# Optimization experiments

Measured on AMD Instinct MI355X. Metric: run time of the kernel, lower is better.

## Reference

```python
import jax, jax.numpy as jnp
import numpy as np

# Model dims
B, S, H, NH = 2, 2048, 1024, 8
HD = H // NH            # head_dim = 128
T = S * NH              # MoE input tokens per batch = 16384
E, K, F = 8, 2, 512     # experts, top_k, expert FFN dim (4*head_dim)


def setup_inputs() -> dict:
    key = jax.random.key(0)
    ks = jax.random.split(key, 9)
    s = 0.02  # init scale
    return {
        "x": jax.random.normal(ks[0], (B, S, H), jnp.float32),
        "W_mh": jax.random.normal(ks[1], (H, H), jnp.float32) * s,
        "b_mh": jnp.zeros((H,), jnp.float32),
        "W_merge": jax.random.normal(ks[2], (H, H), jnp.float32) * s,
        "b_merge": jnp.zeros((H,), jnp.float32),
        "W_router": jax.random.normal(ks[3], (HD, E), jnp.float32) * s,
        "W1": jax.random.normal(ks[4], (E, HD, F), jnp.float32) * s,
        "b1": jnp.zeros((E, F), jnp.float32),
        "W2": jax.random.normal(ks[5], (E, F, HD), jnp.float32) * s,
        "b2": jnp.zeros((E, HD), jnp.float32),
    }


def reference(x, W_mh, b_mh, W_merge, b_merge, W_router, W1, b1, W2, b2):
    # multi-head projection then split heads into the token axis
    h = x @ W_mh + b_mh                       # [B, S, H]
    h = h.reshape(B, T, HD)                   # [B, T, HD]

    # nested VectorizedMoE: top-k token-choice routing over head_dim tokens
    logits = h @ W_router                     # [B, T, E]
    probs = jax.nn.softmax(logits, axis=-1)
    topv, topi = jax.lax.top_k(probs, K)      # [B, T, K]
    topv = topv / jnp.sum(topv, axis=-1, keepdims=True)  # renormalize top-k gates
    # scatter top-k gates into dense [B, T, E] combine weights
    gates = jnp.sum(jax.nn.one_hot(topi, E, dtype=h.dtype) * topv[..., None], axis=-2)

    # vectorized expert FFNs (all experts, combined with sparse gates)
    a = jax.nn.gelu(jnp.einsum('btd,edf->btef', h, W1) + b1)   # [B, T, E, F]
    y = jnp.einsum('btef,efd->bted', a, W2) + b2               # [B, T, E, HD]
    moe_out = jnp.einsum('bte,bted->btd', gates, y)            # [B, T, HD]

    # merge heads back and final projection
    out = moe_out.reshape(B, S, H) @ W_merge + b_merge         # [B, S, H]
    return out
```

## Files before the change

kernel.cpp:

```cpp
#include <hip/hip_runtime.h>


typedef __attribute__((ext_vector_type(8))) short bf16x8;
typedef __attribute__((ext_vector_type(4))) float f32x4;
typedef __attribute__((ext_vector_type(16))) float f32x16;
typedef __attribute__((ext_vector_type(4))) unsigned short u16x4;

constexpr int NSLOT = 66560;
constexpr int NTILE_MAX = 520;
#define CTRL_CNT 0
#define CTRL_CUR 8

__device__ __forceinline__ unsigned short f2bf(float x) {
  unsigned int u = __float_as_uint(x);
  return (unsigned short)((u + 0x7FFFu + ((u >> 16) & 1u)) >> 16);
}
__device__ __forceinline__ float bf2f(unsigned short u) {
  return __uint_as_float(((unsigned int)u) << 16);
}
__device__ __forceinline__ void gload_lds16(const void* g, void* l) {
  __builtin_amdgcn_global_load_lds(
      (const __attribute__((address_space(1))) unsigned int*)g,
      (__attribute__((address_space(3))) unsigned int*)l, 16, 0, 0);
}

__global__ __launch_bounds__(256) void prep_all(
    const float* __restrict__ x, unsigned short* __restrict__ x_bf,
    const float* __restrict__ Wmh, unsigned short* __restrict__ Wmh_t,
    const float* __restrict__ Wmg, unsigned short* __restrict__ Wmg_t,
    const float* __restrict__ W1, const float* __restrict__ W2,
    unsigned short* __restrict__ W1F, unsigned short* __restrict__ W2F,
    const float* __restrict__ bmh, const float* __restrict__ Wr,
    float* __restrict__ Wc, int* __restrict__ ctrl) {
  __shared__ float smem[2048];
  const int bid = blockIdx.x, tid = threadIdx.x;
  if (bid < 1024) {
    if (bid == 0 && tid < 16) ctrl[tid] = 0;
    int i = bid * 256 + tid;
    const int n4 = 4096 * 1024 / 4, stride = 1024 * 256;
    for (; i < n4; i += stride) {
      float4 v = ((const float4*)x)[i];
      u16x4 o;
      o.x = f2bf(v.x); o.y = f2bf(v.y); o.z = f2bf(v.z); o.w = f2bf(v.w);
      ((u16x4*)x_bf)[i] = o;
    }
  } else if (bid < 3072) {
    const int b = bid - 1024;
    const float* src = (b < 1024) ? Wmh : Wmg;
    unsigned short* dst = (b < 1024) ? Wmh_t : Wmg_t;
    const int bb = b & 1023;
    const int c0 = (bb & 31) * 32, r0 = (bb >> 5) * 32;
    const int tx = tid & 31, ty = tid >> 5;
    float (*tile)[33] = (float(*)[33])smem;
    for (int i = ty; i < 32; i += 8)
      tile[i][tx] = src[(size_t)(r0 + i) * 1024 + c0 + tx];
    __syncthreads();
    for (int i = ty; i < 32; i += 8)
      dst[(size_t)(c0 + i) * 1024 + r0 + tx] = f2bf(tile[tx][i]);
  } else if (bid < 3584) {
    const int jid = (bid - 3072) * 4 + (tid >> 6);
    const int l = tid & 63;
    const int is2 = jid >= 1024;
    const int bj = is2 ? jid - 1024 : jid;
    const float* src;
    int C;
    if (!is2) {
      int kk = bj & 7, ft = (bj >> 3) & 15, e = bj >> 7;
      src = W1 + (size_t)e * 65536 + (size_t)(kk * 16) * 512 + ft * 32;
      C = 512;
    } else {
      int sht = bj & 7, ft = (bj >> 3) & 15, e = bj >> 7;
      src = W2 + (size_t)e * 65536 + (size_t)(ft * 32 + (sht >> 2) * 16) * 128 + (sht & 3) * 32;
      C = 128;
    }
    float* tile = smem + (tid >> 6) * 512;
#pragma unroll
    for (int r = 0; r < 8; ++r) {
      int i = l + 64 * r;
      tile[(i >> 5) * 32 + (i & 31)] = src[(size_t)(i >> 5) * C + (i & 31)];
    }
    __syncthreads();
    int l31 = l & 31, lh = l >> 5;
    bf16x8 v;
#pragma unroll
    for (int j = 0; j < 8; ++j) v[j] = (short)f2bf(tile[(lh * 8 + j) * 32 + l31]);
    unsigned short* dst = is2 ? W2F : W1F;
    *(bf16x8*)(dst + ((size_t)bj * 64 + l) * 8) = v;
  } else {
    const int r = (bid - 3584) * 4 + (tid >> 6);
    if (r > 1024) return;
    const int l = tid & 63;
    const float* src = (r < 1024) ? (Wmh + (size_t)r * 1024) : bmh;
    int nh = l >> 3, e = l & 7;
    float acc = 0.f;
    for (int d = 0; d < 128; ++d) acc = fmaf(src[nh * 128 + d], Wr[d * 8 + e], acc);
    Wc[(size_t)r * 64 + l] = acc;
  }
}

__global__ __launch_bounds__(256) void router_kernel(
    const float* __restrict__ x, const float* __restrict__ Wc,
    int* __restrict__ tok_e, float* __restrict__ tok_g,
    int* __restrict__ ctrl, int* __restrict__ perm, float* __restrict__ gateb) {
  int gi = blockIdx.x * 256 + threadIdx.x;
  if (gi < NSLOT) { perm[gi] = 0; gateb[gi] = 0.f; }

  __shared__ float xs[8 * 1024];
  __shared__ float lg[8][64];
  __shared__ int lcnt[8];
  if (threadIdx.x < 8) lcnt[threadIdx.x] = 0;
  int r0 = blockIdx.x * 8;
  const float4* xg = (const float4*)(x + (size_t)r0 * 1024);
  float4* xs4 = (float4*)xs;
  for (int i = threadIdx.x; i < 2048; i += 256) xs4[i] = xg[i];
  __syncthreads();
  int g = threadIdx.x >> 6, lane = threadIdx.x & 63;
  float a0 = Wc[1024 * 64 + lane], a1 = a0;
  const float* x0 = xs + g * 1024;
  const float* x1 = xs + (g + 4) * 1024;
  for (int k = 0; k < 1024; ++k) {
    float w = Wc[(size_t)k * 64 + lane];
    a0 = fmaf(x0[k], w, a0);
    a1 = fmaf(x1[k], w, a1);
  }
  lg[g][lane] = a0; lg[g + 4][lane] = a1;
  __syncthreads();
  if (threadIdx.x < 64) {
    int row = threadIdx.x >> 3, nh = threadIdx.x & 7;
    float l[8];
#pragma unroll
    for (int e = 0; e < 8; ++e) l[e] = lg[row][nh * 8 + e];
    int i1 = 0; float v1 = l[0];
#pragma unroll
    for (int e = 1; e < 8; ++e) if (l[e] > v1) { v1 = l[e]; i1 = e; }
    int i2 = -1; float v2 = -1e30f;
#pragma unroll
    for (int e = 0; e < 8; ++e) if (e != i1 && l[e] > v2) { v2 = l[e]; i2 = e; }
    float g1 = 1.f / (1.f + __expf(v2 - v1));
    float g2 = 1.f - g1;
    size_t t = (size_t)(r0 + row) * 8 + nh;
    tok_e[t * 2] = i1; tok_e[t * 2 + 1] = i2;
    tok_g[t * 2] = g1; tok_g[t * 2 + 1] = g2;
    atomicAdd(&lcnt[i1], 1);
    atomicAdd(&lcnt[i2], 1);
  }
  __syncthreads();
  if (threadIdx.x < 8 && lcnt[threadIdx.x])
    atomicAdd(&ctrl[CTRL_CNT + threadIdx.x], lcnt[threadIdx.x]);
}

__global__ __launch_bounds__(256) void assign_kernel(
    const int* __restrict__ tok_e, const float* __restrict__ tok_g,
    int* __restrict__ ctrl, int* __restrict__ perm,
    float* __restrict__ gateb, int* __restrict__ tok_slot) {
  __shared__ int lcnt[8], lbase[8];
  if (threadIdx.x < 8) lcnt[threadIdx.x] = 0;
  __syncthreads();
  int t = blockIdx.x * 256 + threadIdx.x;
  int e0 = tok_e[t * 2], e1 = tok_e[t * 2 + 1];
  int p0 = atomicAdd(&lcnt[e0], 1);
  int p1 = atomicAdd(&lcnt[e1], 1);
  __syncthreads();
  if (threadIdx.x < 8)
    lbase[threadIdx.x] = atomicAdd(&ctrl[CTRL_CUR + threadIdx.x], lcnt[threadIdx.x]);
  __syncthreads();
  int off0 = 0, off1 = 0, acc = 0;
#pragma unroll
  for (int i = 0; i < 8; ++i) {
    int cnt = ctrl[CTRL_CNT + i];
    if (i == e0) off0 = acc;
    if (i == e1) off1 = acc;
    acc += (cnt + 127) & ~127;
  }
  int s0 = off0 + lbase[e0] + p0;
  int s1 = off1 + lbase[e1] + p1;
  perm[s0] = t; perm[s1] = t;
  gateb[s0] = tok_g[t * 2]; gateb[s1] = tok_g[t * 2 + 1];
  tok_slot[t * 2] = s0; tok_slot[t * 2 + 1] = s1;
}

template <int OUT_BF16>
__global__ __launch_bounds__(256) void gemm_bt(
    const unsigned short* __restrict__ A, const unsigned short* __restrict__ Bt,
    const float* __restrict__ bias, void* __restrict__ Cout,
    int M, int N, int K) {
  __shared__ unsigned short As[2][64 * 64];
  __shared__ unsigned short Bs[2][128 * 64];
  const int tid = threadIdx.x, lane = tid & 63, wid = tid >> 6;
  const int wr = wid & 1, wc = wid >> 1;
  const int m0 = blockIdx.x * 64, n0 = blockIdx.y * 128;
  const int l15 = lane & 15, lhi = lane >> 4;

  f32x4 acc[2][4];
#pragma unroll
  for (int n = 0; n < 4; ++n) {
    float bv = bias[n0 + wc * 64 + n * 16 + l15];
#pragma unroll
    for (int m = 0; m < 2; ++m) acc[m][n] = (f32x4){bv, bv, bv, bv};
  }

  const int rowi = tid >> 3;
  const int segi = (tid & 7) * 8;
  const int NT = K >> 6;

  auto stage = [&](int buf, int kt) {
    const int k0 = kt * 64;
#pragma unroll
    for (int r = 0; r < 2; ++r)
      gload_lds16(A + (size_t)(m0 + r * 32 + rowi) * K + k0 + segi,
                  &As[buf][r * 2048 + wid * 512]);
#pragma unroll
    for (int r = 0; r < 4; ++r)
      gload_lds16(Bt + (size_t)(n0 + r * 32 + rowi) * K + k0 + segi,
                  &Bs[buf][r * 2048 + wid * 512]);
  };

  stage(0, 0);
  asm volatile("s_waitcnt vmcnt(0)" ::: "memory");
  __syncthreads();
  int cur = 0;
  for (int t = 0; t < NT; ++t) {
    if (t + 1 < NT) stage(cur ^ 1, t + 1);
#pragma unroll
    for (int ks = 0; ks < 64; ks += 32) {
      bf16x8 af[2], bb[4];
#pragma unroll
      for (int m = 0; m < 2; ++m)
        af[m] = *(const bf16x8*)&As[cur][(wr * 32 + m * 16 + l15) * 64 + ks + lhi * 8];
#pragma unroll
      for (int n = 0; n < 4; ++n)
        bb[n] = *(const bf16x8*)&Bs[cur][(wc * 64 + n * 16 + l15) * 64 + ks + lhi * 8];
#pragma unroll
      for (int m = 0; m < 2; ++m)
#pragma unroll
        for (int n = 0; n < 4; ++n)
          acc[m][n] = __builtin_amdgcn_mfma_f32_16x16x32_bf16(af[m], bb[n], acc[m][n], 0, 0, 0);
    }
    asm volatile("s_waitcnt vmcnt(0)" ::: "memory");
    __syncthreads();
    cur ^= 1;
  }
#pragma unroll
  for (int m = 0; m < 2; ++m) {
#pragma unroll
    for (int n = 0; n < 4; ++n) {
      int col = n0 + wc * 64 + n * 16 + l15;
#pragma unroll
      for (int j = 0; j < 4; ++j) {
        int row = m0 + wr * 32 + m * 16 + lhi * 4 + j;
        if (OUT_BF16)
          ((unsigned short*)Cout)[(size_t)row * N + col] = f2bf(acc[m][n][j]);
        else
          ((float*)Cout)[(size_t)row * N + col] = acc[m][n][j];
      }
    }
  }
}

__global__ __launch_bounds__(256, 2) void ffn_sparse_v5(
    const unsigned short* __restrict__ hbf,
    const int* __restrict__ ctrl,
    const int* __restrict__ perm,
    const float* __restrict__ gateb,
    const unsigned short* __restrict__ W1F,
    const float* __restrict__ b1,
    const unsigned short* __restrict__ W2F,
    const float* __restrict__ b2,
    unsigned short* __restrict__ ybuf) {
  int e = -1, slotbase = 0;
  {
    int accT = 0, accS = 0;
#pragma unroll
    for (int i = 0; i < 8; ++i) {
      int cnt = ctrl[CTRL_CNT + i];
      int tiles = (cnt + 127) >> 7;
      if (e < 0 && (int)blockIdx.x < accT + tiles) {
        e = i;
        slotbase = accS + ((int)blockIdx.x - accT) * 128;
      }
      accT += tiles;
      accS += tiles * 128;
    }
  }
  if (e < 0) return;

  const int tid = threadIdx.x, l = tid & 63, w = tid >> 6;
  const int l31 = l & 31, lh = l >> 5;
  const int slot = slotbase + w * 32 + l31;
  const int prow = perm[slot];
  const float gate = gateb[slot];

  bf16x8 hreg[8];
  const unsigned short* hsrc = hbf + (size_t)prow * 128 + lh * 8;
#pragma unroll
  for (int kk = 0; kk < 8; ++kk)
    hreg[kk] = *(const bf16x8*)(hsrc + kk * 16);

  const unsigned short* W1e = W1F + (size_t)e * 65536 + l * 8;
  const unsigned short* W2e = W2F + (size_t)e * 65536 + l * 8;
  const float4* b14 = (const float4*)(b1 + (size_t)e * 512);

  f32x16 yacc[4] = {};
  for (int it = 0; it < 8; ++it) {
    bf16x8 w1c[16], w2a[8], w2b[8];
#pragma unroll
    for (int i = 0; i < 16; ++i)
      w1c[i] = *(const bf16x8*)(W1e + (size_t)it * 8192 + i * 512);
#pragma unroll
    for (int i = 0; i < 8; ++i)
      w2a[i] = *(const bf16x8*)(W2e + (size_t)it * 8192 + i * 512);
    float4 p0 = b14[it * 16 + lh],     p1 = b14[it * 16 + lh + 2];
    float4 p2 = b14[it * 16 + lh + 4], p3 = b14[it * 16 + lh + 6];
    float4 q0 = b14[it * 16 + 8 + lh],     q1 = b14[it * 16 + 8 + lh + 2];
    float4 q2 = b14[it * 16 + 8 + lh + 4], q3 = b14[it * 16 + 8 + lh + 6];
    f32x16 a0 = {p0.x, p0.y, p0.z, p0.w, p1.x, p1.y, p1.z, p1.w,
                 p2.x, p2.y, p2.z, p2.w, p3.x, p3.y, p3.z, p3.w};
    f32x16 a1 = {q0.x, q0.y, q0.z, q0.w, q1.x, q1.y, q1.z, q1.w,
                 q2.x, q2.y, q2.z, q2.w, q3.x, q3.y, q3.z, q3.w};
#pragma unroll
    for (int kk = 0; kk < 8; ++kk) {
      a0 = __builtin_amdgcn_mfma_f32_32x32x16_bf16(w1c[kk], hreg[kk], a0, 0, 0, 0);
      a1 = __builtin_amdgcn_mfma_f32_32x32x16_bf16(w1c[8 + kk], hreg[kk], a1, 0, 0, 0);
    }
#pragma unroll
    for (int i = 0; i < 8; ++i)
      w2b[i] = *(const bf16x8*)(W2e + (size_t)it * 8192 + 4096 + i * 512);
    float ge0[16], ge1[16];
#pragma unroll
    for (int r = 0; r < 16; ++r) {
      float v = a0[r];
      float s2 = v * v;
      float q = fmaf(0.1029432f, s2, 2.3022078f);
      float E = exp2f(v * q);
      float rc = __builtin_amdgcn_rcpf(E + 1.f);
      ge0[r] = fmaf(-v, rc, v) * gate;
      float v1 = a1[r];
      float s21 = v1 * v1;
      float q1v = fmaf(0.1029432f, s21, 2.3022078f);
      float E1 = exp2f(v1 * q1v);
      float rc1 = __builtin_amdgcn_rcpf(E1 + 1.f);
      ge1[r] = fmaf(-v1, rc1, v1) * gate;
    }
    unsigned pk0[8], pk1[8];
#pragma unroll
    for (int p = 0; p < 8; ++p) {
      unsigned r0v, r1v;
      asm("v_cvt_pk_bf16_f32 %0, %1, %2" : "=v"(r0v) : "v"(ge0[2 * p]), "v"(ge0[2 * p + 1]));
      asm("v_cvt_pk_bf16_f32 %0, %1, %2" : "=v"(r1v) : "v"(ge1[2 * p]), "v"(ge1[2 * p + 1]));
      pk0[p] = r0v; pk1[p] = r1v;
    }
    asm volatile("v_permlane32_swap_b32 %0, %1" : "+v"(pk0[0]), "+v"(pk0[2]));
    asm volatile("v_permlane32_swap_b32 %0, %1" : "+v"(pk0[1]), "+v"(pk0[3]));
    asm volatile("v_permlane32_swap_b32 %0, %1" : "+v"(pk0[4]), "+v"(pk0[6]));
    asm volatile("v_permlane32_swap_b32 %0, %1" : "+v"(pk0[5]), "+v"(pk0[7]));
    asm volatile("v_permlane32_swap_b32 %0, %1" : "+v"(pk1[0]), "+v"(pk1[2]));
    asm volatile("v_permlane32_swap_b32 %0, %1" : "+v"(pk1[1]), "+v"(pk1[3]));
    asm volatile("v_permlane32_swap_b32 %0, %1" : "+v"(pk1[4]), "+v"(pk1[6]));
    asm volatile("v_permlane32_swap_b32 %0, %1" : "+v"(pk1[5]), "+v"(pk1[7]));
    typedef __attribute__((ext_vector_type(4))) unsigned u32x4;
    u32x4 f00 = {pk0[0], pk0[1], pk0[2], pk0[3]};
    u32x4 f01 = {pk0[4], pk0[5], pk0[6], pk0[7]};
    u32x4 f10 = {pk1[0], pk1[1], pk1[2], pk1[3]};
    u32x4 f11 = {pk1[4], pk1[5], pk1[6], pk1[7]};
    bf16x8 act00 = __builtin_bit_cast(bf16x8, f00);
    bf16x8 act01 = __builtin_bit_cast(bf16x8, f01);
    bf16x8 act10 = __builtin_bit_cast(bf16x8, f10);
    bf16x8 act11 = __builtin_bit_cast(bf16x8, f11);
#pragma unroll
    for (int ht = 0; ht < 4; ++ht) {
      yacc[ht] = __builtin_amdgcn_mfma_f32_32x32x16_bf16(w2a[ht], act00, yacc[ht], 0, 0, 0);
      yacc[ht] = __builtin_amdgcn_mfma_f32_32x32x16_bf16(w2a[4 + ht], act01, yacc[ht], 0, 0, 0);
      yacc[ht] = __builtin_amdgcn_mfma_f32_32x32x16_bf16(w2b[ht], act10, yacc[ht], 0, 0, 0);
      yacc[ht] = __builtin_amdgcn_mfma_f32_32x32x16_bf16(w2b[4 + ht], act11, yacc[ht], 0, 0, 0);
    }
  }
  const float* b2e = b2 + (size_t)e * 128;
#pragma unroll
  for (int ht = 0; ht < 4; ++ht) {
#pragma unroll
    for (int rp = 0; rp < 8; ++rp) {
      int fr = ((2 * rp) & 3) + 8 * (rp >> 1) + 4 * lh;
      int hd = ht * 32 + fr;
      float2 bb2 = *(const float2*)&b2e[hd];
      float v0 = fmaf(gate, bb2.x, yacc[ht][2 * rp]);
      float v1 = fmaf(gate, bb2.y, yacc[ht][2 * rp + 1]);
      unsigned pw;
      asm("v_cvt_pk_bf16_f32 %0, %1, %2" : "=v"(pw) : "v"(v0), "v"(v1));
      *(unsigned*)(ybuf + (size_t)slot * 128 + hd) = pw;
    }
  }
}

__global__ __launch_bounds__(256) void combine_kernel(
    const unsigned short* __restrict__ ybuf, const int* __restrict__ tok_slot,
    unsigned short* __restrict__ moebf) {
  int t = blockIdx.x * 8 + (threadIdx.x >> 5);
  int c = (threadIdx.x & 31) * 4;
  int s0 = tok_slot[t * 2], s1 = tok_slot[t * 2 + 1];
  u16x4 a = *(const u16x4*)(ybuf + (size_t)s0 * 128 + c);
  u16x4 b = *(const u16x4*)(ybuf + (size_t)s1 * 128 + c);
  u16x4 o;
#pragma unroll
  for (int i = 0; i < 4; ++i) o[i] = f2bf(bf2f(a[i]) + bf2f(b[i]));
  *(u16x4*)(moebf + (size_t)t * 128 + c) = o;
}

extern "C" void kernel_launch(void* const* d_in, const int* in_sizes, int n_in,
                              void* d_out, int out_size, void* d_ws, size_t ws_size,
                              hipStream_t stream) {
  const float* x       = (const float*)d_in[0];
  const float* W_mh    = (const float*)d_in[1];
  const float* b_mh    = (const float*)d_in[2];
  const float* W_merge = (const float*)d_in[3];
  const float* b_merge = (const float*)d_in[4];
  const float* W_rout  = (const float*)d_in[5];
  const float* W1      = (const float*)d_in[6];
  const float* b1      = (const float*)d_in[7];
  const float* W2      = (const float*)d_in[8];
  const float* b2      = (const float*)d_in[9];
  float* out = (float*)d_out;

  char* ws = (char*)d_ws;
  size_t off = 0;
  auto alloc = [&](size_t bytes) {
    void* p = ws + off;
    off = (off + bytes + 255) & ~(size_t)255;
    return p;
  };
  unsigned short* x_bf  = (unsigned short*)alloc((size_t)4096 * 1024 * 2);
  unsigned short* Wmh_t = (unsigned short*)alloc((size_t)1024 * 1024 * 2);
  unsigned short* Wmg_t = (unsigned short*)alloc((size_t)1024 * 1024 * 2);
  unsigned short* W1F   = (unsigned short*)alloc((size_t)8 * 512 * 128 * 2);
  unsigned short* W2F   = (unsigned short*)alloc((size_t)8 * 512 * 128 * 2);
  unsigned short* h_bf  = (unsigned short*)alloc((size_t)4096 * 1024 * 2);
  unsigned short* moebf = (unsigned short*)alloc((size_t)4096 * 1024 * 2);
  unsigned short* ybuf  = (unsigned short*)alloc((size_t)NSLOT * 128 * 2);
  float* Wc             = (float*)alloc((size_t)1025 * 64 * 4);
  int*   ctrl           = (int*)alloc(4096);
  int*   tok_e          = (int*)alloc((size_t)32768 * 2 * 4);
  float* tok_g          = (float*)alloc((size_t)32768 * 2 * 4);
  int*   tok_slot       = (int*)alloc((size_t)32768 * 2 * 4);
  int*   perm           = (int*)alloc((size_t)NSLOT * 4);
  float* gateb          = (float*)alloc((size_t)NSLOT * 4);

  prep_all<<<3841, 256, 0, stream>>>(x, x_bf, W_mh, Wmh_t, W_merge, Wmg_t,
                                     W1, W2, W1F, W2F, b_mh, W_rout, Wc, ctrl);
  router_kernel<<<512, 256, 0, stream>>>(x, Wc, tok_e, tok_g, ctrl, perm, gateb);
  assign_kernel<<<128, 256, 0, stream>>>(tok_e, tok_g, ctrl, perm, gateb, tok_slot);
  gemm_bt<1><<<dim3(64, 8), 256, 0, stream>>>(x_bf, Wmh_t, b_mh, (void*)h_bf, 4096, 1024, 1024);
  ffn_sparse_v5<<<NTILE_MAX, 256, 0, stream>>>(h_bf, ctrl, perm, gateb, W1F, b1, W2F, b2, ybuf);
  combine_kernel<<<4096, 256, 0, stream>>>(ybuf, tok_slot, moebf);
  gemm_bt<0><<<dim3(64, 8), 256, 0, stream>>>(moebf, Wmg_t, b_merge, (void*)out, 4096, 1024, 1024);
}
```

Measured before the change: 166.7 us.

## Stage expert weights in LDS with double buffering and split F across wave groups

The sparse FFN kernel moves from 256 to 512 threads per block. Two wave groups each handle half of the F dimension and combine their partial outputs through an LDS reduction at the end. Expert W1/W2 chunks are now loaded into double-buffered shared memory with direct global-to-LDS loads, prefetching the next chunk while the current one is computed, instead of every wave loading its own copy into registers. This removes redundant global weight traffic and register pressure, and doubles the waves available to hide latency. In exchange it adds per-iteration barriers, LDS footprint and an extra reduction step.

Measured after the change: 176.7 us. +6.0%, slower.

```diff
diff --git a/kernel.cpp b/kernel.cpp
--- a/kernel.cpp
+++ b/kernel.cpp
@@ -257,7 +257,7 @@
   }
 }
 
-__global__ __launch_bounds__(256, 2) void ffn_sparse_v5(
+__global__ __launch_bounds__(512, 4) void ffn_sparse_v6(
     const unsigned short* __restrict__ hbf,
     const int* __restrict__ ctrl,
     const int* __restrict__ perm,
@@ -284,109 +284,127 @@
   }
   if (e < 0) return;
 
+  __shared__ __align__(16) unsigned short pool[32768];
+  unsigned short* W1s = pool;
+  unsigned short* W2s = pool + 16384;
+  float* yred = (float*)pool;
+
   const int tid = threadIdx.x, l = tid & 63, w = tid >> 6;
   const int l31 = l & 31, lh = l >> 5;
-  const int slot = slotbase + w * 32 + l31;
+  const int fh = w >> 2, ws = w & 3;
+  const int slot = slotbase + ws * 32 + l31;
   const int prow = perm[slot];
   const float gate = gateb[slot];
 
   bf16x8 hreg[8];
-  const unsigned short* hsrc = hbf + (size_t)prow * 128 + lh * 8;
-#pragma unroll
-  for (int kk = 0; kk < 8; ++kk)
-    hreg[kk] = *(const bf16x8*)(hsrc + kk * 16);
-
-  const unsigned short* W1e = W1F + (size_t)e * 65536 + l * 8;
-  const unsigned short* W2e = W2F + (size_t)e * 65536 + l * 8;
+  {
+    const unsigned short* hsrc = hbf + (size_t)prow * 128 + lh * 8;
+#pragma unroll
+    for (int kk = 0; kk < 8; ++kk)
+      hreg[kk] = *(const bf16x8*)(hsrc + kk * 16);
+  }
+
+  const unsigned short* W1e = W1F + (size_t)e * 65536;
+  const unsigned short* W2e = W2F + (size_t)e * 65536;
   const float4* b14 = (const float4*)(b1 + (size_t)e * 512);
 
+  auto stage = [&](int buf, int ft) {
+#pragma unroll
+    for (int r = 0; r < 2; ++r) {
+      gload_lds16(W1e + (size_t)ft * 4096 + (size_t)(r * 256 + ws * 64 + l) * 8,
+                  W1s + (fh * 2 + buf) * 4096 + (r * 256 + ws * 64) * 8);
+      gload_lds16(W2e + (size_t)ft * 4096 + (size_t)(r * 256 + ws * 64 + l) * 8,
+                  W2s + (fh * 2 + buf) * 4096 + (r * 256 + ws * 64) * 8);
+    }
+  };
+
+  stage(0, fh * 8);
+  asm volatile("s_waitcnt vmcnt(0)" ::: "memory");
+  __syncthreads();
+
   f32x16 yacc[4] = {};
+  int cur = 0;
   for (int it = 0; it < 8; ++it) {
-    bf16x8 w1c[16], w2a[8], w2b[8];
-#pragma unroll
-    for (int i = 0; i < 16; ++i)
-      w1c[i] = *(const bf16x8*)(W1e + (size_t)it * 8192 + i * 512);
-#pragma unroll
-    for (int i = 0; i < 8; ++i)
-      w2a[i] = *(const bf16x8*)(W2e + (size_t)it * 8192 + i * 512);
-    float4 p0 = b14[it * 16 + lh],     p1 = b14[it * 16 + lh + 2];
-    float4 p2 = b14[it * 16 + lh + 4], p3 = b14[it * 16 + lh + 6];
-    float4 q0 = b14[it * 16 + 8 + lh],     q1 = b14[it * 16 + 8 + lh + 2];
-    float4 q2 = b14[it * 16 + 8 + lh + 4], q3 = b14[it * 16 + 8 + lh + 6];
-    f32x16 a0 = {p0.x, p0.y, p0.z, p0.w, p1.x, p1.y, p1.z, p1.w,
-                 p2.x, p2.y, p2.z, p2.w, p3.x, p3.y, p3.z, p3.w};
-    f32x16 a1 = {q0.x, q0.y, q0.z, q0.w, q1.x, q1.y, q1.z, q1.w,
-                 q2.x, q2.y, q2.z, q2.w, q3.x, q3.y, q3.z, q3.w};
+    const int ft = fh * 8 + it;
+    if (it < 7) stage(cur ^ 1, ft + 1);
+    float4 q0 = b14[ft * 8 + lh],     q1 = b14[ft * 8 + lh + 2];
+    float4 q2 = b14[ft * 8 + lh + 4], q3 = b14[ft * 8 + lh + 6];
+    f32x16 aacc = {q0.x, q0.y, q0.z, q0.w, q1.x, q1.y, q1.z, q1.w,
+                   q2.x, q2.y, q2.z, q2.w, q3.x, q3.y, q3.z, q3.w};
+    const unsigned short* W1c = W1s + (fh * 2 + cur) * 4096;
 #pragma unroll
     for (int kk = 0; kk < 8; ++kk) {
-      a0 = __builtin_amdgcn_mfma_f32_32x32x16_bf16(w1c[kk], hreg[kk], a0, 0, 0, 0);
-      a1 = __builtin_amdgcn_mfma_f32_32x32x16_bf16(w1c[8 + kk], hreg[kk], a1, 0, 0, 0);
-    }
-#pragma unroll
-    for (int i = 0; i < 8; ++i)
-      w2b[i] = *(const bf16x8*)(W2e + (size_t)it * 8192 + 4096 + i * 512);
-    float ge0[16], ge1[16];
+      bf16x8 a1 = *(const bf16x8*)(W1c + (kk * 64 + l) * 8);
+      aacc = __builtin_amdgcn_mfma_f32_32x32x16_bf16(a1, hreg[kk], aacc, 0, 0, 0);
+    }
+    float ge[16];
 #pragma unroll
     for (int r = 0; r < 16; ++r) {
-      float v = a0[r];
+      float v = aacc[r];
       float s2 = v * v;
       float q = fmaf(0.1029432f, s2, 2.3022078f);
       float E = exp2f(v * q);
       float rc = __builtin_amdgcn_rcpf(E + 1.f);
-      ge0[r] = fmaf(-v, rc, v) * gate;
-      float v1 = a1[r];
-      float s21 = v1 * v1;
-      float q1v = fmaf(0.1029432f, s21, 2.3022078f);
-      float E1 = exp2f(v1 * q1v);
-      float rc1 = __builtin_amdgcn_rcpf(E1 + 1.f);
-      ge1[r] = fmaf(-v1, rc1, v1) * gate;
-    }
-    unsigned pk0[8], pk1[8];
+      ge[r] = fmaf(-v, rc, v) * gate;
+    }
+    unsigned pk[8];
 #pragma unroll
     for (int p = 0; p < 8; ++p) {
-      unsigned r0v, r1v;
-      asm("v_cvt_pk_bf16_f32 %0, %1, %2" : "=v"(r0v) : "v"(ge0[2 * p]), "v"(ge0[2 * p + 1]));
-      asm("v_cvt_pk_bf16_f32 %0, %1, %2" : "=v"(r1v) : "v"(ge1[2 * p]), "v"(ge1[2 * p + 1]));
-      pk0[p] = r0v; pk1[p] = r1v;
-    }
-    asm volatile("v_permlane32_swap_b32 %0, %1" : "+v"(pk0[0]), "+v"(pk0[2]));
-    asm volatile("v_permlane32_swap_b32 %0, %1" : "+v"(pk0[1]), "+v"(pk0[3]));
-    asm volatile("v_permlane32_swap_b32 %0, %1" : "+v"(pk0[4]), "+v"(pk0[6]));
-    asm volatile("v_permlane32_swap_b32 %0, %1" : "+v"(pk0[5]), "+v"(pk0[7]));
-    asm volatile("v_permlane32_swap_b32 %0, %1" : "+v"(pk1[0]), "+v"(pk1[2]));
-    asm volatile("v_permlane32_swap_b32 %0, %1" : "+v"(pk1[1]), "+v"(pk1[3]));
-    asm volatile("v_permlane32_swap_b32 %0, %1" : "+v"(pk1[4]), "+v"(pk1[6]));
-    asm volatile("v_permlane32_swap_b32 %0, %1" : "+v"(pk1[5]), "+v"(pk1[7]));
+      unsigned r;
+      asm("v_cvt_pk_bf16_f32 %0, %1, %2" : "=v"(r) : "v"(ge[2 * p]), "v"(ge[2 * p + 1]));
+      pk[p] = r;
+    }
+    asm volatile("v_permlane32_swap_b32 %0, %1" : "+v"(pk[0]), "+v"(pk[2]));
+    asm volatile("v_permlane32_swap_b32 %0, %1" : "+v"(pk[1]), "+v"(pk[3]));
+    asm volatile("v_permlane32_swap_b32 %0, %1" : "+v"(pk[4]), "+v"(pk[6]));
+    asm volatile("v_permlane32_swap_b32 %0, %1" : "+v"(pk[5]), "+v"(pk[7]));
     typedef __attribute__((ext_vector_type(4))) unsigned u32x4;
-    u32x4 f00 = {pk0[0], pk0[1], pk0[2], pk0[3]};
-    u32x4 f01 = {pk0[4], pk0[5], pk0[6], pk0[7]};
-    u32x4 f10 = {pk1[0], pk1[1], pk1[2], pk1[3]};
-    u32x4 f11 = {pk1[4], pk1[5], pk1[6], pk1[7]};
-    bf16x8 act00 = __builtin_bit_cast(bf16x8, f00);
-    bf16x8 act01 = __builtin_bit_cast(bf16x8, f01);
-    bf16x8 act10 = __builtin_bit_cast(bf16x8, f10);
-    bf16x8 act11 = __builtin_bit_cast(bf16x8, f11);
+    u32x4 f0 = {pk[0], pk[1], pk[2], pk[3]};
+    u32x4 f1 = {pk[4], pk[5], pk[6], pk[7]};
+    bf16x8 act0 = __builtin_bit_cast(bf16x8, f0);
+    bf16x8 act1 = __builtin_bit_cast(bf16x8, f1);
+    const unsigned short* W2c = W2s + (fh * 2 + cur) * 4096;
 #pragma unroll
     for (int ht = 0; ht < 4; ++ht) {
-      yacc[ht] = __builtin_amdgcn_mfma_f32_32x32x16_bf16(w2a[ht], act00, yacc[ht], 0, 0, 0);
-      yacc[ht] = __builtin_amdgcn_mfma_f32_32x32x16_bf16(w2a[4 + ht], act01, yacc[ht], 0, 0, 0);
-      yacc[ht] = __builtin_amdgcn_mfma_f32_32x32x16_bf16(w2b[ht], act10, yacc[ht], 0, 0, 0);
-      yacc[ht] = __builtin_amdgcn_mfma_f32_32x32x16_bf16(w2b[4 + ht], act11, yacc[ht], 0, 0, 0);
-    }
-  }
-  const float* b2e = b2 + (size_t)e * 128;
-#pragma unroll
-  for (int ht = 0; ht < 4; ++ht) {
-#pragma unroll
-    for (int rp = 0; rp < 8; ++rp) {
-      int fr = ((2 * rp) & 3) + 8 * (rp >> 1) + 4 * lh;
-      int hd = ht * 32 + fr;
-      float2 bb2 = *(const float2*)&b2e[hd];
-      float v0 = fmaf(gate, bb2.x, yacc[ht][2 * rp]);
-      float v1 = fmaf(gate, bb2.y, yacc[ht][2 * rp + 1]);
-      unsigned pw;
-      asm("v_cvt_pk_bf16_f32 %0, %1, %2" : "=v"(pw) : "v"(v0), "v"(v1));
-      *(unsigned*)(ybuf + (size_t)slot * 128 + hd) = pw;
+      bf16x8 a20 = *(const bf16x8*)(W2c + (ht * 64 + l) * 8);
+      yacc[ht] = __builtin_amdgcn_mfma_f32_32x32x16_bf16(a20, act0, yacc[ht], 0, 0, 0);
+      bf16x8 a21 = *(const bf16x8*)(W2c + ((4 + ht) * 64 + l) * 8);
+      yacc[ht] = __builtin_amdgcn_mfma_f32_32x32x16_bf16(a21, act1, yacc[ht], 0, 0, 0);
+    }
+    asm volatile("s_waitcnt vmcnt(0)" ::: "memory");
+    __syncthreads();
+    cur ^= 1;
+  }
+
+  const int sl = ws * 32 + l31;
+  if (fh == 1) {
+#pragma unroll
+    for (int ht = 0; ht < 4; ++ht) {
+#pragma unroll
+      for (int rp = 0; rp < 8; ++rp) {
+        int fr = ((2 * rp) & 3) + 8 * (rp >> 1) + 4 * lh;
+        int hd = ht * 32 + fr;
+        yred[hd * 128 + sl] = yacc[ht][2 * rp];
+        yred[(hd + 1) * 128 + sl] = yacc[ht][2 * rp + 1];
+      }
+    }
+  }
+  __syncthreads();
+  if (fh == 0) {
+    const float* b2e = b2 + (size_t)e * 128;
+#pragma unroll
+    for (int ht = 0; ht < 4; ++ht) {
+#pragma unroll
+      for (int rp = 0; rp < 8; ++rp) {
+        int fr = ((2 * rp) & 3) + 8 * (rp >> 1) + 4 * lh;
+        int hd = ht * 32 + fr;
+        float2 bb2 = *(const float2*)&b2e[hd];
+        float v0 = yacc[ht][2 * rp] + yred[hd * 128 + sl] + gate * bb2.x;
+        float v1 = yacc[ht][2 * rp + 1] + yred[(hd + 1) * 128 + sl] + gate * bb2.y;
+        unsigned pw;
+        asm("v_cvt_pk_bf16_f32 %0, %1, %2" : "=v"(pw) : "v"(v0), "v"(v1));
+        *(unsigned*)(ybuf + (size_t)slot * 128 + hd) = pw;
+      }
     }
   }
 }
@@ -448,7 +466,7 @@
   router_kernel<<<512, 256, 0, stream>>>(x, Wc, tok_e, tok_g, ctrl, perm, gateb);
   assign_kernel<<<128, 256, 0, stream>>>(tok_e, tok_g, ctrl, perm, gateb, tok_slot);
   gemm_bt<1><<<dim3(64, 8), 256, 0, stream>>>(x_bf, Wmh_t, b_mh, (void*)h_bf, 4096, 1024, 1024);
-  ffn_sparse_v5<<<NTILE_MAX, 256, 0, stream>>>(h_bf, ctrl, perm, gateb, W1F, b1, W2F, b2, ybuf);
+  ffn_sparse_v6<<<NTILE_MAX, 512, 0, stream>>>(h_bf, ctrl, perm, gateb, W1F, b1, W2F, b2, ybuf);
   combine_kernel<<<4096, 256, 0, stream>>>(ybuf, tok_slot, moebf);
   gemm_bt<0><<<dim3(64, 8), 256, 0, stream>>>(moebf, Wmg_t, b_merge, (void*)out, 4096, 1024, 1024);
 }
```

## Stage expert FFN weights through double-buffered LDS with async global-to-LDS loads

Applied to the files above, without the earlier changes.

In the sparse expert FFN kernel, each wave used to load its own copy of the W1/W2 chunks from global memory into registers. Now the block cooperatively stages each iteration's chunks into double-buffered shared memory using global_load_lds, prefetching the next chunk while the current one is consumed. MFMA sections are raised with s_setprio, and the gate multiply moves from every activation to the final output. This cuts redundant global traffic and register pressure across the four waves, at the cost of about 64KB of LDS per block and a barrier each iteration, which may limit occupancy.

Result: faster. 163.0 us (-2.2%).

```diff
diff --git a/kernel.cpp b/kernel.cpp
--- a/kernel.cpp
+++ b/kernel.cpp
@@ -257,7 +257,7 @@
   }
 }
 
-__global__ __launch_bounds__(256, 2) void ffn_sparse_v5(
+__global__ __launch_bounds__(256, 2) void ffn_sparse_v7(
     const unsigned short* __restrict__ hbf,
     const int* __restrict__ ctrl,
     const int* __restrict__ perm,
@@ -284,6 +284,9 @@
   }
   if (e < 0) return;
 
+  __shared__ __align__(16) unsigned short W1c[2][2][4096];
+  __shared__ __align__(16) unsigned short W2c[2][2][4096];
+
   const int tid = threadIdx.x, l = tid & 63, w = tid >> 6;
   const int l31 = l & 31, lh = l >> 5;
   const int slot = slotbase + w * 32 + l31;
@@ -291,40 +294,57 @@
   const float gate = gateb[slot];
 
   bf16x8 hreg[8];
-  const unsigned short* hsrc = hbf + (size_t)prow * 128 + lh * 8;
-#pragma unroll
-  for (int kk = 0; kk < 8; ++kk)
-    hreg[kk] = *(const bf16x8*)(hsrc + kk * 16);
-
-  const unsigned short* W1e = W1F + (size_t)e * 65536 + l * 8;
-  const unsigned short* W2e = W2F + (size_t)e * 65536 + l * 8;
+  {
+    const unsigned short* hsrc = hbf + (size_t)prow * 128 + lh * 8;
+#pragma unroll
+    for (int kk = 0; kk < 8; ++kk)
+      hreg[kk] = *(const bf16x8*)(hsrc + kk * 16);
+  }
+
+  const unsigned short* W1e = W1F + (size_t)e * 65536;
+  const unsigned short* W2e = W2F + (size_t)e * 65536;
   const float4* b14 = (const float4*)(b1 + (size_t)e * 512);
 
+  auto stage = [&](int buf, int it) {
+#pragma unroll
+    for (int f2 = 0; f2 < 2; ++f2) {
+      const int ft = it * 2 + f2;
+#pragma unroll
+      for (int r = 0; r < 2; ++r) {
+        gload_lds16(W1e + (size_t)ft * 4096 + (size_t)(r * 256 + tid) * 8,
+                    &W1c[buf][f2][r * 2048 + w * 512]);
+        gload_lds16(W2e + (size_t)ft * 4096 + (size_t)(r * 256 + tid) * 8,
+                    &W2c[buf][f2][r * 2048 + w * 512]);
+      }
+    }
+  };
+
+  stage(0, 0);
+  asm volatile("s_waitcnt vmcnt(0)" ::: "memory");
+  __syncthreads();
+
   f32x16 yacc[4] = {};
+  int cur = 0;
   for (int it = 0; it < 8; ++it) {
-    bf16x8 w1c[16], w2a[8], w2b[8];
-#pragma unroll
-    for (int i = 0; i < 16; ++i)
-      w1c[i] = *(const bf16x8*)(W1e + (size_t)it * 8192 + i * 512);
-#pragma unroll
-    for (int i = 0; i < 8; ++i)
-      w2a[i] = *(const bf16x8*)(W2e + (size_t)it * 8192 + i * 512);
-    float4 p0 = b14[it * 16 + lh],     p1 = b14[it * 16 + lh + 2];
-    float4 p2 = b14[it * 16 + lh + 4], p3 = b14[it * 16 + lh + 6];
-    float4 q0 = b14[it * 16 + 8 + lh],     q1 = b14[it * 16 + 8 + lh + 2];
-    float4 q2 = b14[it * 16 + 8 + lh + 4], q3 = b14[it * 16 + 8 + lh + 6];
+    const int ft0 = it * 2, ft1 = it * 2 + 1;
+    if (it < 7) stage(cur ^ 1, it + 1);
+    float4 p0 = b14[ft0 * 8 + lh],     p1 = b14[ft0 * 8 + lh + 2];
+    float4 p2 = b14[ft0 * 8 + lh + 4], p3 = b14[ft0 * 8 + lh + 6];
+    float4 q0 = b14[ft1 * 8 + lh],     q1 = b14[ft1 * 8 + lh + 2];
+    float4 q2 = b14[ft1 * 8 + lh + 4], q3 = b14[ft1 * 8 + lh + 6];
     f32x16 a0 = {p0.x, p0.y, p0.z, p0.w, p1.x, p1.y, p1.z, p1.w,
                  p2.x, p2.y, p2.z, p2.w, p3.x, p3.y, p3.z, p3.w};
     f32x16 a1 = {q0.x, q0.y, q0.z, q0.w, q1.x, q1.y, q1.z, q1.w,
                  q2.x, q2.y, q2.z, q2.w, q3.x, q3.y, q3.z, q3.w};
+    __builtin_amdgcn_s_setprio(1);
 #pragma unroll
     for (int kk = 0; kk < 8; ++kk) {
-      a0 = __builtin_amdgcn_mfma_f32_32x32x16_bf16(w1c[kk], hreg[kk], a0, 0, 0, 0);
-      a1 = __builtin_amdgcn_mfma_f32_32x32x16_bf16(w1c[8 + kk], hreg[kk], a1, 0, 0, 0);
-    }
-#pragma unroll
-    for (int i = 0; i < 8; ++i)
-      w2b[i] = *(const bf16x8*)(W2e + (size_t)it * 8192 + 4096 + i * 512);
+      bf16x8 w10 = *(const bf16x8*)&W1c[cur][0][(kk * 64 + l) * 8];
+      bf16x8 w11 = *(const bf16x8*)&W1c[cur][1][(kk * 64 + l) * 8];
+      a0 = __builtin_amdgcn_mfma_f32_32x32x16_bf16(w10, hreg[kk], a0, 0, 0, 0);
+      a1 = __builtin_amdgcn_mfma_f32_32x32x16_bf16(w11, hreg[kk], a1, 0, 0, 0);
+    }
+    __builtin_amdgcn_s_setprio(0);
     float ge0[16], ge1[16];
 #pragma unroll
     for (int r = 0; r < 16; ++r) {
@@ -333,13 +353,13 @@
       float q = fmaf(0.1029432f, s2, 2.3022078f);
       float E = exp2f(v * q);
       float rc = __builtin_amdgcn_rcpf(E + 1.f);
-      ge0[r] = fmaf(-v, rc, v) * gate;
+      ge0[r] = fmaf(-v, rc, v);
       float v1 = a1[r];
       float s21 = v1 * v1;
       float q1v = fmaf(0.1029432f, s21, 2.3022078f);
       float E1 = exp2f(v1 * q1v);
       float rc1 = __builtin_amdgcn_rcpf(E1 + 1.f);
-      ge1[r] = fmaf(-v1, rc1, v1) * gate;
+      ge1[r] = fmaf(-v1, rc1, v1);
     }
     unsigned pk0[8], pk1[8];
 #pragma unroll
@@ -366,13 +386,22 @@
     bf16x8 act01 = __builtin_bit_cast(bf16x8, f01);
     bf16x8 act10 = __builtin_bit_cast(bf16x8, f10);
     bf16x8 act11 = __builtin_bit_cast(bf16x8, f11);
+    __builtin_amdgcn_s_setprio(1);
 #pragma unroll
     for (int ht = 0; ht < 4; ++ht) {
-      yacc[ht] = __builtin_amdgcn_mfma_f32_32x32x16_bf16(w2a[ht], act00, yacc[ht], 0, 0, 0);
-      yacc[ht] = __builtin_amdgcn_mfma_f32_32x32x16_bf16(w2a[4 + ht], act01, yacc[ht], 0, 0, 0);
-      yacc[ht] = __builtin_amdgcn_mfma_f32_32x32x16_bf16(w2b[ht], act10, yacc[ht], 0, 0, 0);
-      yacc[ht] = __builtin_amdgcn_mfma_f32_32x32x16_bf16(w2b[4 + ht], act11, yacc[ht], 0, 0, 0);
-    }
+      bf16x8 b00 = *(const bf16x8*)&W2c[cur][0][(ht * 64 + l) * 8];
+      bf16x8 b01 = *(const bf16x8*)&W2c[cur][0][((4 + ht) * 64 + l) * 8];
+      bf16x8 b10 = *(const bf16x8*)&W2c[cur][1][(ht * 64 + l) * 8];
+      bf16x8 b11 = *(const bf16x8*)&W2c[cur][1][((4 + ht) * 64 + l) * 8];
+      yacc[ht] = __builtin_amdgcn_mfma_f32_32x32x16_bf16(b00, act00, yacc[ht], 0, 0, 0);
+      yacc[ht] = __builtin_amdgcn_mfma_f32_32x32x16_bf16(b01, act01, yacc[ht], 0, 0, 0);
+      yacc[ht] = __builtin_amdgcn_mfma_f32_32x32x16_bf16(b10, act10, yacc[ht], 0, 0, 0);
+      yacc[ht] = __builtin_amdgcn_mfma_f32_32x32x16_bf16(b11, act11, yacc[ht], 0, 0, 0);
+    }
+    __builtin_amdgcn_s_setprio(0);
+    asm volatile("s_waitcnt vmcnt(0)" ::: "memory");
+    __syncthreads();
+    cur ^= 1;
   }
   const float* b2e = b2 + (size_t)e * 128;
 #pragma unroll
@@ -382,8 +411,8 @@
       int fr = ((2 * rp) & 3) + 8 * (rp >> 1) + 4 * lh;
       int hd = ht * 32 + fr;
       float2 bb2 = *(const float2*)&b2e[hd];
-      float v0 = fmaf(gate, bb2.x, yacc[ht][2 * rp]);
-      float v1 = fmaf(gate, bb2.y, yacc[ht][2 * rp + 1]);
+      float v0 = gate * (yacc[ht][2 * rp] + bb2.x);
+      float v1 = gate * (yacc[ht][2 * rp + 1] + bb2.y);
       unsigned pw;
       asm("v_cvt_pk_bf16_f32 %0, %1, %2" : "=v"(pw) : "v"(v0), "v"(v1));
       *(unsigned*)(ybuf + (size_t)slot * 128 + hd) = pw;
@@ -448,7 +477,7 @@
   router_kernel<<<512, 256, 0, stream>>>(x, Wc, tok_e, tok_g, ctrl, perm, gateb);
   assign_kernel<<<128, 256, 0, stream>>>(tok_e, tok_g, ctrl, perm, gateb, tok_slot);
   gemm_bt<1><<<dim3(64, 8), 256, 0, stream>>>(x_bf, Wmh_t, b_mh, (void*)h_bf, 4096, 1024, 1024);
-  ffn_sparse_v5<<<NTILE_MAX, 256, 0, stream>>>(h_bf, ctrl, perm, gateb, W1F, b1, W2F, b2, ybuf);
+  ffn_sparse_v7<<<NTILE_MAX, 256, 0, stream>>>(h_bf, ctrl, perm, gateb, W1F, b1, W2F, b2, ybuf);
   combine_kernel<<<4096, 256, 0, stream>>>(ybuf, tok_slot, moebf);
   gemm_bt<0><<<dim3(64, 8), 256, 0, stream>>>(moebf, Wmg_t, b_merge, (void*)out, 4096, 1024, 1024);
 }
```
